# Kernel optimization log

Measured on AMD Instinct MI355X. Metric: run time of the kernel, lower is better.

## Reference

```python
import jax, jax.numpy as jnp
import numpy as np
from jax import lax

B, S, T = 512, 256, 10      # batch, src len, max_len (decoder steps)
V, E, H = 28, 32, 128       # vocab, embed, hidden
PAD = 0


def setup_inputs():
    key = jax.random.key(0)
    ks = jax.random.split(key, 16)
    k = 1.0 / np.sqrt(H)

    def u(kk, shape):
        return jax.random.uniform(kk, shape, jnp.float32, -k, k)

    embed = jax.random.normal(ks[0], (V, E), jnp.float32) * 0.02
    embed = embed.at[PAD].set(0.0)  # padding_idx=0 row is zero
    return dict(
        src=jax.random.randint(ks[1], (B, S), 0, V),
        target=jax.random.randint(ks[2], (B, T), 0, V),
        embed=embed,
        # PyTorch LSTM bias b = b_ih + b_hh folded into one vector (same math)
        enc_Wih_f=u(ks[3], (4 * H, E)), enc_Whh_f=u(ks[4], (4 * H, H)), enc_b_f=u(ks[5], (4 * H,)),
        enc_Wih_b=u(ks[6], (4 * H, E)), enc_Whh_b=u(ks[7], (4 * H, H)), enc_b_b=u(ks[8], (4 * H,)),
        dec_Wih=u(ks[9], (4 * H, E)), dec_Whh=u(ks[10], (4 * H, H)), dec_b=u(ks[11], (4 * H,)),
        proj_W=u(ks[12], (H, 2 * H)), proj_b=jnp.zeros((H,), jnp.float32),
        attn_W=u(ks[13], (H, 2 * H)), attn_b=jnp.zeros((H,), jnp.float32),
        out_W=u(ks[14], (V, H)), out_b=jnp.zeros((V,), jnp.float32),
    )


def _cell(h, c, xg, Whh):
    # PyTorch LSTMCell gate order: i, f, g, o
    g = xg + h @ Whh.T
    i, f, gg, o = jnp.split(g, 4, axis=-1)
    c = jax.nn.sigmoid(f) * c + jax.nn.sigmoid(i) * jnp.tanh(gg)
    return jax.nn.sigmoid(o) * jnp.tanh(c), c


def _run_lstm(x_emb, Wih, Whh, b):
    # precompute input projections for all steps: [S, B, 4H]
    xg = jnp.einsum('bse,ge->sbg', x_emb, Wih) + b
    h0 = jnp.zeros((x_emb.shape[0], Whh.shape[1]), x_emb.dtype)

    def step(carry, xg_t):
        h, c = _cell(carry[0], carry[1], xg_t, Whh)
        return (h, c), h

    (h, c), hs = lax.scan(step, (h0, h0), xg)
    return jnp.transpose(hs, (1, 0, 2)), h, c  # [B,S,H], [B,H], [B,H]


def _forward(src, target, embed, enc_Wih_f, enc_Whh_f, enc_b_f,
             enc_Wih_b, enc_Whh_b, enc_b_b, dec_Wih, dec_Whh, dec_b,
             proj_W, proj_b, attn_W, attn_b, out_W, out_b):
    src_emb = embed[src]  # [B,S,E]
    hs_f, hf, cf = _run_lstm(src_emb, enc_Wih_f, enc_Whh_f, enc_b_f)
    hs_r, hb, cb = _run_lstm(src_emb[:, ::-1], enc_Wih_b, enc_Whh_b, enc_b_b)
    enc_out = jnp.concatenate([hs_f, hs_r[:, ::-1]], axis=-1)  # [B,S,2H]
    h0, c0 = hf + hb, cf + cb  # sum over directions (num_layers=1)
    enc_proj = jnp.einsum('bsd,hd->bsh', enc_out, proj_W) + proj_b  # [B,S,H]

    # teacher forcing with ratio=1.0: decoder input tokens = [PAD, target[:, :-1]]
    dec_tok = jnp.concatenate(
        [jnp.full((src.shape[0], 1), PAD, target.dtype), target[:, :T - 1]], axis=1)
    xg_dec = jnp.einsum('bte,ge->tbg', embed[dec_tok], dec_Wih) + dec_b  # [T,B,4H]

    def dstep(carry, xg_t):
        h, c = _cell(carry[0], carry[1], xg_t, dec_Whh)
        scores = jnp.einsum('bsh,bh->bs', enc_proj, h)
        aw = jax.nn.softmax(scores, axis=1)
        ctx = jnp.einsum('bs,bsh->bh', aw, enc_proj)
        comb = jnp.tanh(jnp.concatenate([h, ctx], axis=1) @ attn_W.T + attn_b)
        logits = comb @ out_W.T + out_b
        return (h, c), logits

    _, logits = lax.scan(dstep, (h0, c0), xg_dec)  # [T,B,V]
    return jnp.transpose(logits, (1, 0, 2))  # [B,T,V]


def reference(src, target, embed, enc_Wih_f, enc_Whh_f, enc_b_f,
              enc_Wih_b, enc_Whh_b, enc_b_b, dec_Wih, dec_Whh, dec_b,
              proj_W, proj_b, attn_W, attn_b, out_W, out_b):
    return _forward(src, target, embed, enc_Wih_f, enc_Whh_f, enc_b_f,
                    enc_Wih_b, enc_Whh_b, enc_b_b, dec_Wih, dec_Whh, dec_b,
                    proj_W, proj_b, attn_W, attn_b, out_W, out_b)
```

## Files before the change

kernel.cpp:

```cpp
#include <hip/hip_runtime.h>
#include <hip/hip_bf16.h>
#include <stdint.h>

typedef unsigned short ushort_t;
typedef unsigned int uint_t;
typedef __attribute__((ext_vector_type(8))) short bfrag;
typedef __attribute__((ext_vector_type(4))) float f32x4;

#define B_ 512
#define S_ 256
#define T_ 10
#define V_ 28
#define H_ 128

#define XTD 0
#define XTG 14336
#define WTD 43008
#define AWT 108544
#define OWT 141312
#define PWT 144896
#define WPK 177664
#define HFIN 308736
#define CFIN 439808
#define HDEC 570880
#define HS_BYTE_OFF (1226240ull * 4ull)
#define PREP_N 308736

__device__ __forceinline__ float fast_exp2(float x) { return __builtin_amdgcn_exp2f(x); }
__device__ __forceinline__ float fast_rcp(float x)  { return __builtin_amdgcn_rcpf(x); }
__device__ __forceinline__ float sigm(float x) {
    return fast_rcp(1.f + fast_exp2(-1.4426950408889634f * x));
}
__device__ __forceinline__ float tanh_(float x) {
    return 1.f - 2.f * fast_rcp(1.f + fast_exp2(2.8853900817779268f * x));
}
__device__ __forceinline__ ushort_t f2bf(float x) {
    uint_t u = __float_as_uint(x);
    return (ushort_t)((u + 0x7FFFu + ((u >> 16) & 1u)) >> 16);
}
__device__ __forceinline__ float bflo(uint_t u) { return __uint_as_float(u << 16); }
__device__ __forceinline__ float bfhi(uint_t u) { return __uint_as_float(u & 0xFFFF0000u); }

__device__ __forceinline__ void lds_barrier() {
    asm volatile("s_waitcnt lgkmcnt(0)" ::: "memory");
    __builtin_amdgcn_s_barrier();
    __builtin_amdgcn_sched_barrier(0);
}

__global__ __launch_bounds__(256) void prep_kernel(
    const float* __restrict__ embed,
    const float* __restrict__ Wih_f, const float* __restrict__ b_f,
    const float* __restrict__ Wih_b, const float* __restrict__ b_b,
    const float* __restrict__ Wih_d, const float* __restrict__ b_d,
    const float* __restrict__ Whh_f, const float* __restrict__ Whh_b,
    const float* __restrict__ Whh_d,
    const float* __restrict__ attn_W, const float* __restrict__ out_W,
    const float* __restrict__ proj_W,
    float* __restrict__ ws)
{
    int i = blockIdx.x * 256 + threadIdx.x;
    if (i < XTG) {
        int v = i >> 9, q = i & 511;
        int uu = q >> 2, g = q & 3;
        int jj = g * 128 + uu;
        float acc = b_d[jj];
        #pragma unroll
        for (int e = 0; e < 32; ++e) acc = fmaf(embed[v * 32 + e], Wih_d[jj * 32 + e], acc);
        ws[XTD + i] = acc;
    } else if (i < WTD) {
        int r = i - XTG; int d = r / 14336; int rem = r % 14336;
        int v = rem >> 9, q = rem & 511;
        int uu = q >> 2, g = q & 3;
        int jj = g * 128 + uu;
        const float* Wih = d ? Wih_b : Wih_f;
        const float* bb  = d ? b_b   : b_f;
        float acc = bb[jj];
        #pragma unroll
        for (int e = 0; e < 32; ++e) acc = fmaf(embed[v * 32 + e], Wih[jj * 32 + e], acc);
        ws[XTG + r] = acc;
    } else if (i < AWT) {
        ws[i] = 0.f;
    } else if (i < OWT) {
        int r = i - AWT; int k = r >> 7, uu = r & 127;
        ws[i] = attn_W[uu * 256 + k];
    } else if (i < PWT) {
        int r = i - OWT; int k = r / 28, v = r % 28;
        ws[i] = out_W[v * 128 + k];
    } else if (i < WPK) {
        int r = i - PWT; int k = r >> 7, uu = r & 127;
        ws[i] = proj_W[uu * 256 + k];
    } else {
        int i2 = (i - WPK) * 2;
        #pragma unroll
        for (int p = 0; p < 2; ++p, ++i2) {
            if (i2 < 131072) {
                int e  = i2 & 7;
                int ll = (i2 >> 3) & 63;
                int kt = (i2 >> 9) & 3;
                int ni = (i2 >> 11) & 3;
                int wv = (i2 >> 13) & 7;
                int d  = (i2 >> 16) & 1;
                int jj = (ni * 8 + wv) * 16 + (ll & 15);
                int kp = kt * 32 + ((ll >> 4) << 3) + e;
                const float* Whh = d ? Whh_b : Whh_f;
                ((ushort_t*)(ws + WPK))[i2] = f2bf(Whh[jj * 128 + kp]);
            } else if (i2 < 196608) {
                int j2 = i2 - 131072;
                int e  = j2 & 7;
                int ll = (j2 >> 3) & 63;
                int kt = (j2 >> 9) & 3;
                int ni = (j2 >> 11) & 3;
                int wv = (j2 >> 13) & 7;
                int jj = (ni * 8 + wv) * 16 + (ll & 15);
                int kp = kt * 32 + ((ll >> 4) << 3) + e;
                ((ushort_t*)(ws + WPK))[i2] = f2bf(Whh_d[jj * 128 + kp]);
            }
        }
    }
}

__global__ __launch_bounds__(512, 2) void enc_kernel(
    const int* __restrict__ src,
    const float* __restrict__ xtg_base,
    const ushort_t* __restrict__ wpk,
    float* __restrict__ hfin, float* __restrict__ cfin,
    ushort_t* __restrict__ hs)
{
    const int bx = blockIdx.x;
    const int dir = bx >> 7;
    const int b0 = (bx & 127) << 2;
    const int tid = threadIdx.x;
    const int w = tid >> 6, l = tid & 63;
    const int lg = l >> 4, col = l & 15;
    const int u = (w << 4) + col;
    const int row = lg;

    __shared__ __align__(16) ushort_t hb[2][4][144];
    __shared__ __align__(16) int tokl[256][4];

    for (int i = tid; i < 1024; i += 512)
        tokl[i >> 2][i & 3] = src[(b0 + (i & 3)) * S_ + (i >> 2)];
    for (int i = tid; i < 576; i += 512) ((uint_t*)hb)[i] = 0u;

    const float* xtg = xtg_base + dir * 14336;

    bfrag bf[4][4];
    {
        const ushort_t* wb = wpk + (((size_t)dir * 8 + w) << 13) + l * 8;
        #pragma unroll
        for (int ni = 0; ni < 4; ++ni)
            #pragma unroll
            for (int kt = 0; kt < 4; ++kt)
                bf[ni][kt] = *reinterpret_cast<const bfrag*>(wb + ((ni * 4 + kt) << 9));
    }
    __syncthreads();

    float c_reg = 0.f, h_reg = 0.f;

    f32x4 xg_cur, xg_next;
    {
        int p0 = dir ? (S_ - 1) : 0;
        xg_cur = *reinterpret_cast<const f32x4*>(xtg + ((size_t)tokl[p0][row] << 9) + (u << 2));
    }

    const bfrag zf = {0, 0, 0, 0, 0, 0, 0, 0};
    bfrag af0 = zf, af1 = zf, af2 = zf, af3 = zf;
    const bool ard = ((col & 3) == 0);
    const int ar = col >> 2;
    const int swz = ar << 3;
    const f32x4 zacc = {0.f, 0.f, 0.f, 0.f};

    ushort_t* hs_ptr = hs + ((size_t)(b0 + row) * S_ + (dir ? (S_ - 1) : 0)) * 256
                          + dir * 128 + u;
    const int hs_step = dir ? -256 : 256;

    for (int t = 0; t < S_; ++t) {
        const int cb = t & 1, nb = cb ^ 1;

        if (t + 1 < S_) {
            int pn = dir ? (S_ - 2 - t) : (t + 1);
            xg_next = *reinterpret_cast<const f32x4*>(xtg + ((size_t)tokl[pn][row] << 9) + (u << 2));
        }

        if (ard) {
            const ushort_t* hp = &hb[cb][ar][0];
            af0 = *reinterpret_cast<const bfrag*>(hp + ((  0 + (lg << 3)) ^ swz));
            af1 = *reinterpret_cast<const bfrag*>(hp + (( 32 + (lg << 3)) ^ swz));
            af2 = *reinterpret_cast<const bfrag*>(hp + (( 64 + (lg << 3)) ^ swz));
            af3 = *reinterpret_cast<const bfrag*>(hp + (( 96 + (lg << 3)) ^ swz));
        }

        f32x4 a0 = __builtin_amdgcn_mfma_f32_16x16x32_bf16(af0, bf[0][0], zacc, 0, 0, 0);
        f32x4 a1 = __builtin_amdgcn_mfma_f32_16x16x32_bf16(af0, bf[1][0], zacc, 0, 0, 0);
        f32x4 a2 = __builtin_amdgcn_mfma_f32_16x16x32_bf16(af0, bf[2][0], zacc, 0, 0, 0);
        f32x4 a3 = __builtin_amdgcn_mfma_f32_16x16x32_bf16(af0, bf[3][0], zacc, 0, 0, 0);
        #define KT1(AF, kt) { \
            a0 = __builtin_amdgcn_mfma_f32_16x16x32_bf16(AF, bf[0][kt], a0, 0, 0, 0); \
            a1 = __builtin_amdgcn_mfma_f32_16x16x32_bf16(AF, bf[1][kt], a1, 0, 0, 0); \
            a2 = __builtin_amdgcn_mfma_f32_16x16x32_bf16(AF, bf[2][kt], a2, 0, 0, 0); \
            a3 = __builtin_amdgcn_mfma_f32_16x16x32_bf16(AF, bf[3][kt], a3, 0, 0, 0); \
        }
        KT1(af1, 1) KT1(af2, 2) KT1(af3, 3)
        #undef KT1

        {
            float gi = a0[0] + xg_cur[0], gf = a1[0] + xg_cur[1];
            float gg = a2[0] + xg_cur[2], go = a3[0] + xg_cur[3];
            float ii = sigm(gi), ff = sigm(gf), gG = tanh_(gg), oo = sigm(go);
            c_reg = ff * c_reg + ii * gG;
            float h = oo * tanh_(c_reg);
            h_reg = h;
            ushort_t hi = f2bf(h);
            hb[nb][row][u ^ (row << 3)] = hi;
            *hs_ptr = hi;
            hs_ptr += hs_step;
        }
        xg_cur = xg_next;
        lds_barrier();
    }

    hfin[dir * 65536 + (b0 + row) * 128 + u] = h_reg;
    cfin[dir * 65536 + (b0 + row) * 128 + u] = c_reg;
}

__global__ __launch_bounds__(512, 2) void dec_kernel(
    const int* __restrict__ target,
    const float* __restrict__ xtd_gi,
    const ushort_t* __restrict__ wpk,
    const float* __restrict__ hfin, const float* __restrict__ cfin,
    float* __restrict__ hdec)
{
    const int b0 = blockIdx.x << 2;
    const int tid = threadIdx.x;
    const int w = tid >> 6, l = tid & 63;
    const int lg = l >> 4, col = l & 15;
    const int u = (w << 4) + col;
    const int row = lg;

    __shared__ __align__(16) ushort_t hb[2][4][144];
    __shared__ __align__(16) int tokl[T_][4];

    if (tid < 40) {
        int t = tid >> 2, r = tid & 3;
        tokl[t][r] = (t == 0) ? 0 : target[(b0 + r) * T_ + t - 1];
    }

    bfrag bf[4][4];
    {
        const ushort_t* wb = wpk + 131072 + ((size_t)w << 13) + l * 8;
        #pragma unroll
        for (int ni = 0; ni < 4; ++ni)
            #pragma unroll
            for (int kt = 0; kt < 4; ++kt)
                bf[ni][kt] = *reinterpret_cast<const bfrag*>(wb + ((ni * 4 + kt) << 9));
    }

    float c_reg, h_reg;
    {
        int gb = (b0 + row) * 128 + u;
        h_reg = hfin[gb] + hfin[65536 + gb];
        c_reg = cfin[gb] + cfin[65536 + gb];
        hb[0][row][u ^ (row << 3)] = f2bf(h_reg);
    }
    __syncthreads();

    const bfrag zf = {0, 0, 0, 0, 0, 0, 0, 0};
    bfrag af0 = zf, af1 = zf, af2 = zf, af3 = zf;
    const bool ard = ((col & 3) == 0);
    const int ar = col >> 2;
    const int swz = ar << 3;
    const f32x4 zacc = {0.f, 0.f, 0.f, 0.f};

    for (int t = 0; t < T_; ++t) {
        const int cb = t & 1, nb = cb ^ 1;

        f32x4 xgc = *reinterpret_cast<const f32x4*>(
            xtd_gi + ((size_t)tokl[t][row] << 9) + (u << 2));

        if (ard) {
            const ushort_t* hp = &hb[cb][ar][0];
            af0 = *reinterpret_cast<const bfrag*>(hp + ((  0 + (lg << 3)) ^ swz));
            af1 = *reinterpret_cast<const bfrag*>(hp + (( 32 + (lg << 3)) ^ swz));
            af2 = *reinterpret_cast<const bfrag*>(hp + (( 64 + (lg << 3)) ^ swz));
            af3 = *reinterpret_cast<const bfrag*>(hp + (( 96 + (lg << 3)) ^ swz));
        }

        f32x4 a0 = __builtin_amdgcn_mfma_f32_16x16x32_bf16(af0, bf[0][0], zacc, 0, 0, 0);
        f32x4 a1 = __builtin_amdgcn_mfma_f32_16x16x32_bf16(af0, bf[1][0], zacc, 0, 0, 0);
        f32x4 a2 = __builtin_amdgcn_mfma_f32_16x16x32_bf16(af0, bf[2][0], zacc, 0, 0, 0);
        f32x4 a3 = __builtin_amdgcn_mfma_f32_16x16x32_bf16(af0, bf[3][0], zacc, 0, 0, 0);
        #define KT1(AF, kt) { \
            a0 = __builtin_amdgcn_mfma_f32_16x16x32_bf16(AF, bf[0][kt], a0, 0, 0, 0); \
            a1 = __builtin_amdgcn_mfma_f32_16x16x32_bf16(AF, bf[1][kt], a1, 0, 0, 0); \
            a2 = __builtin_amdgcn_mfma_f32_16x16x32_bf16(AF, bf[2][kt], a2, 0, 0, 0); \
            a3 = __builtin_amdgcn_mfma_f32_16x16x32_bf16(AF, bf[3][kt], a3, 0, 0, 0); \
        }
        KT1(af1, 1) KT1(af2, 2) KT1(af3, 3)
        #undef KT1

        {
            float gi = a0[0] + xgc[0], gf = a1[0] + xgc[1];
            float gg = a2[0] + xgc[2], go = a3[0] + xgc[3];
            float ii = sigm(gi), ff = sigm(gf), gG = tanh_(gg), oo = sigm(go);
            c_reg = ff * c_reg + ii * gG;
            float h = oo * tanh_(c_reg);
            h_reg = h;
            hb[nb][row][u ^ (row << 3)] = f2bf(h);
            hdec[((size_t)(b0 + row) * T_ + t) * 128 + u] = h;
        }
        lds_barrier();
    }
}

#define ESW(unit, row) ((((unit) ^ ((row) & 31))) << 3)
__global__ __launch_bounds__(512, 1) void attn_kernel(
    const float* __restrict__ hdec,
    const float* __restrict__ projW, const float* __restrict__ proj_b,
    const float* __restrict__ projWT,
    const float* __restrict__ attn_WT, const float* __restrict__ attn_b,
    const float* __restrict__ out_WT, const float* __restrict__ out_b,
    const ushort_t* __restrict__ hs, float* __restrict__ out)
{
    const int b = blockIdx.x;
    const int tid = threadIdx.x;

    __shared__ __align__(16) char smem[156672];
    ushort_t* e_lds = (ushort_t*)smem;
    float* hd   = (float*)(smem + 131072);
    float* q    = (float*)(smem + 136192);
    float* sc   = (float*)(smem + 146432);
    float* part = (float*)smem;
    float* wsum = (float*)(smem + 40960);

    const ushort_t* e = hs + (size_t)b * 65536;

    uint4 st[16];
    #pragma unroll
    for (int i = 0; i < 16; ++i)
        st[i] = *reinterpret_cast<const uint4*>(e + (i * 512 + tid) * 8);

    for (int i = tid; i < 1280; i += 512) hd[i] = hdec[(size_t)b * 1280 + i];
    lds_barrier();

    {
        const int half = tid >> 8, d = tid & 255;
        float acc[5];
        #pragma unroll
        for (int i = 0; i < 5; ++i) acc[i] = 0.f;
        for (int k = 0; k < 128; ++k) {
            float pw = projW[k * 256 + d];
            #pragma unroll
            for (int i = 0; i < 5; ++i) acc[i] = fmaf(hd[(half * 5 + i) * 128 + k], pw, acc[i]);
        }
        int swd = d ^ ((((uint_t)d >> 5) & 7) << 2);
        #pragma unroll
        for (int i = 0; i < 5; ++i) q[(half * 5 + i) * 256 + swd] = acc[i];
    }

    #pragma unroll
    for (int i = 0; i < 16; ++i) {
        int idx = i * 512 + tid;
        int row = idx >> 5, c = idx & 31;
        *reinterpret_cast<uint4*>(e_lds + row * 256 + ESW(c, row)) = st[i];
    }
    lds_barrier();

    {
        const int w = tid >> 6, l = tid & 63;
        const int s3 = l >> 3, k8 = l & 7;
        uint4 E0[4], E1[4], E2[4], E3[4];
        #pragma unroll
        for (int p = 0; p < 4; ++p) {
            int s = w * 32 + p * 8 + s3;
            const ushort_t* lrow = e_lds + s * 256;
            E0[p] = *reinterpret_cast<const uint4*>(lrow + ESW((k8 << 2) + 0, s));
            E1[p] = *reinterpret_cast<const uint4*>(lrow + ESW((k8 << 2) + 1, s));
            E2[p] = *reinterpret_cast<const uint4*>(lrow + ESW((k8 << 2) + 2, s));
            E3[p] = *reinterpret_cast<const uint4*>(lrow + ESW((k8 << 2) + 3, s));
        }
        for (int t = 0; t < 10; ++t) {
            const float* qb = &q[t * 256];
            #define QCH(i) (*reinterpret_cast<const float4*>(&qb[(k8 * 32 + (i) * 4) ^ (k8 << 2)]))
            float4 Q0 = QCH(0), Q1 = QCH(1), Q2 = QCH(2), Q3 = QCH(3);
            float4 Q4 = QCH(4), Q5 = QCH(5), Q6 = QCH(6), Q7 = QCH(7);
            #undef QCH
            #pragma unroll
            for (int p = 0; p < 4; ++p) {
                float a = 0.f;
                #define DOT4(pa, pb, qv) { float4 q_ = (qv); \
                    a = fmaf(bflo(pa), q_.x, a); a = fmaf(bfhi(pa), q_.y, a); \
                    a = fmaf(bflo(pb), q_.z, a); a = fmaf(bfhi(pb), q_.w, a); }
                DOT4(E0[p].x, E0[p].y, Q0); DOT4(E0[p].z, E0[p].w, Q1);
                DOT4(E1[p].x, E1[p].y, Q2); DOT4(E1[p].z, E1[p].w, Q3);
                DOT4(E2[p].x, E2[p].y, Q4); DOT4(E2[p].z, E2[p].w, Q5);
                DOT4(E3[p].x, E3[p].y, Q6); DOT4(E3[p].z, E3[p].w, Q7);
                #undef DOT4
                a += __shfl_xor(a, 1);
                a += __shfl_xor(a, 2);
                a += __shfl_xor(a, 4);
                if (k8 == 0) sc[t * 256 + (w * 32 + p * 8 + s3)] = a;
            }
        }
    }
    __syncthreads();

    {
        const int w = tid >> 6, l = tid & 63;
        for (int t = w; t < 10; t += 8) {
            float4 sv = *reinterpret_cast<const float4*>(&sc[t * 256 + l * 4]);
            float m = fmaxf(fmaxf(sv.x, sv.y), fmaxf(sv.z, sv.w));
            #pragma unroll
            for (int o = 1; o < 64; o <<= 1) m = fmaxf(m, __shfl_xor(m, o));
            float e0 = fast_exp2((sv.x - m) * 1.4426950408889634f);
            float e1 = fast_exp2((sv.y - m) * 1.4426950408889634f);
            float e2 = fast_exp2((sv.z - m) * 1.4426950408889634f);
            float e3 = fast_exp2((sv.w - m) * 1.4426950408889634f);
            float ssum = e0 + e1 + e2 + e3;
            #pragma unroll
            for (int o = 1; o < 64; o <<= 1) ssum += __shfl_xor(ssum, o);
            float inv = fast_rcp(ssum);
            *reinterpret_cast<float4*>(&sc[t * 256 + l * 4]) =
                make_float4(e0 * inv, e1 * inv, e2 * inv, e3 * inv);
        }
    }
    __syncthreads();

    {
        const int w = tid >> 6, l = tid & 63;
        const int chunk = w >> 1, tH = (w & 1) * 5;
        const int sbase = chunk * 64;
        const int unit = l >> 1, half2 = (l & 1) << 2;
        float ax[5], ay[5], az[5], aw2[5];
        #pragma unroll
        for (int i = 0; i < 5; ++i) { ax[i] = 0.f; ay[i] = 0.f; az[i] = 0.f; aw2[i] = 0.f; }
        for (int c4 = 0; c4 < 16; ++c4) {
            int s0 = sbase + c4 * 4;
            uint2 eA = *reinterpret_cast<const uint2*>(e_lds + (s0 + 0) * 256 + ESW(unit, s0 + 0) + half2);
            uint2 eB = *reinterpret_cast<const uint2*>(e_lds + (s0 + 1) * 256 + ESW(unit, s0 + 1) + half2);
            uint2 eC = *reinterpret_cast<const uint2*>(e_lds + (s0 + 2) * 256 + ESW(unit, s0 + 2) + half2);
            uint2 eD = *reinterpret_cast<const uint2*>(e_lds + (s0 + 3) * 256 + ESW(unit, s0 + 3) + half2);
            #pragma unroll
            for (int i = 0; i < 5; ++i) {
                float4 a4 = *reinterpret_cast<const float4*>(&sc[(tH + i) * 256 + s0]);
                ax[i]  = fmaf(bflo(eA.x), a4.x, ax[i]);  ay[i]  = fmaf(bfhi(eA.x), a4.x, ay[i]);
                az[i]  = fmaf(bflo(eA.y), a4.x, az[i]);  aw2[i] = fmaf(bfhi(eA.y), a4.x, aw2[i]);
                ax[i]  = fmaf(bflo(eB.x), a4.y, ax[i]);  ay[i]  = fmaf(bfhi(eB.x), a4.y, ay[i]);
                az[i]  = fmaf(bflo(eB.y), a4.y, az[i]);  aw2[i] = fmaf(bfhi(eB.y), a4.y, aw2[i]);
                ax[i]  = fmaf(bflo(eC.x), a4.z, ax[i]);  ay[i]  = fmaf(bfhi(eC.x), a4.z, ay[i]);
                az[i]  = fmaf(bflo(eC.y), a4.z, az[i]);  aw2[i] = fmaf(bfhi(eC.y), a4.z, aw2[i]);
                ax[i]  = fmaf(bflo(eD.x), a4.w, ax[i]);  ay[i]  = fmaf(bfhi(eD.x), a4.w, ay[i]);
                az[i]  = fmaf(bflo(eD.y), a4.w, az[i]);  aw2[i] = fmaf(bfhi(eD.y), a4.w, aw2[i]);
            }
        }
        __syncthreads();
        #pragma unroll
        for (int i = 0; i < 5; ++i)
            *reinterpret_cast<float4*>(&part[(chunk * 10 + tH + i) * 256 + l * 4]) =
                make_float4(ax[i], ay[i], az[i], aw2[i]);
    }
    __syncthreads();

    for (int i = tid; i < 2560; i += 512)
        wsum[i] = part[i] + part[2560 + i] + part[5120 + i] + part[7680 + i];
    if (tid < 512) wsum[2560 + tid] = 0.f;
    __syncthreads();

    {
        const int u = tid & 127, th = tid >> 7;
        const int st5 = (th < 2) ? th * 3 : 6 + (th - 2) * 2;
        const int cn = (th < 2) ? 3 : 2;
        float acc[3];
        #pragma unroll
        for (int i = 0; i < 3; ++i) acc[i] = proj_b[u];
        for (int k = 0; k < 256; ++k) {
            float pw = projWT[k * 128 + u];
            #pragma unroll
            for (int i = 0; i < 3; ++i) acc[i] = fmaf(pw, wsum[(st5 + i) * 256 + k], acc[i]);
        }
        #pragma unroll
        for (int i = 0; i < 3; ++i)
            if (i < cn) q[(st5 + i) * 128 + u] = acc[i];
    }
    __syncthreads();

    {
        const int u = tid & 127, th = tid >> 7;
        const int st6 = (th < 2) ? th * 3 : 6 + (th - 2) * 2;
        const int cn = (th < 2) ? 3 : 2;
        float acc[3];
        #pragma unroll
        for (int i = 0; i < 3; ++i) acc[i] = attn_b[u];
        for (int k = 0; k < 128; ++k) {
            float a1 = attn_WT[k * 128 + u];
            #pragma unroll
            for (int i = 0; i < 3; ++i) {
                int tt = (st6 + i < 10) ? (st6 + i) : 9;
                acc[i] = fmaf(a1, hd[tt * 128 + k], acc[i]);
            }
        }
        for (int k = 0; k < 128; ++k) {
            float a2 = attn_WT[(128 + k) * 128 + u];
            #pragma unroll
            for (int i = 0; i < 3; ++i) {
                int tt = (st6 + i < 10) ? (st6 + i) : 9;
                acc[i] = fmaf(a2, q[tt * 128 + k], acc[i]);
            }
        }
        #pragma unroll
        for (int i = 0; i < 3; ++i)
            if (i < cn) q[1280 + (st6 + i) * 128 + u] = tanh_(acc[i]);
    }
    __syncthreads();

    for (int o = tid; o < 280; o += 512) {
        int t = o / 28, v = o - t * 28;
        float acc = out_b[v];
        #pragma unroll 4
        for (int k = 0; k < 128; ++k)
            acc = fmaf(out_WT[k * 28 + v], q[1280 + t * 128 + k], acc);
        out[(size_t)b * 280 + o] = acc;
    }
}

extern "C" void kernel_launch(void* const* d_in, const int* in_sizes, int n_in,
                              void* d_out, int out_size, void* d_ws, size_t ws_size,
                              hipStream_t stream) {
    const int* src      = (const int*)d_in[0];
    const int* target   = (const int*)d_in[1];
    const float* embed  = (const float*)d_in[2];
    const float* Wih_f  = (const float*)d_in[3];
    const float* Whh_f  = (const float*)d_in[4];
    const float* b_f    = (const float*)d_in[5];
    const float* Wih_b  = (const float*)d_in[6];
    const float* Whh_b  = (const float*)d_in[7];
    const float* b_b    = (const float*)d_in[8];
    const float* Wih_d  = (const float*)d_in[9];
    const float* Whh_d  = (const float*)d_in[10];
    const float* b_d    = (const float*)d_in[11];
    const float* proj_W = (const float*)d_in[12];
    const float* proj_b = (const float*)d_in[13];
    const float* attn_W = (const float*)d_in[14];
    const float* attn_b = (const float*)d_in[15];
    const float* out_W  = (const float*)d_in[16];
    const float* out_b  = (const float*)d_in[17];

    float* ws = (float*)d_ws;
    ushort_t* hs = (ushort_t*)((char*)d_ws + HS_BYTE_OFF);
    float* out = (float*)d_out;

    prep_kernel<<<(PREP_N + 255) / 256, 256, 0, stream>>>(
        embed, Wih_f, b_f, Wih_b, b_b, Wih_d, b_d,
        Whh_f, Whh_b, Whh_d, attn_W, out_W, proj_W, ws);

    enc_kernel<<<256, 512, 0, stream>>>(
        src, ws + XTG, (const ushort_t*)(ws + WPK),
        ws + HFIN, ws + CFIN, hs);

    dec_kernel<<<128, 512, 0, stream>>>(
        target, ws + XTD, (const ushort_t*)(ws + WPK),
        ws + HFIN, ws + CFIN, ws + HDEC);

    attn_kernel<<<512, 512, 0, stream>>>(
        ws + HDEC, proj_W, proj_b, ws + PWT, ws + AWT, attn_b,
        ws + OWT, out_b, hs, out);
}
```

Before: 264.6 us.

## Precompute LDS fragment pointers, raise MFMA priority, fuse attn h-half into projection loop

In the encoder recurrence, the swizzled LDS read and write addresses for both double-buffer halves are computed once before the loop and chosen per step with a select. The MFMA chain is wrapped in s_setprio so the wave gets issue priority during the matmul. In the attention tail, the h-half of the attn_W product is folded into the projection loop and stored in an sc buffer, so the next phase only runs the ctx half. This trades extra registers and a new LDS buffer for less address arithmetic and fewer serial loop passes.

Result: faster. 254.6 us (-3.8%).

```diff
diff --git a/kernel.cpp b/kernel.cpp
--- a/kernel.cpp
+++ b/kernel.cpp
@@ -170,12 +170,22 @@
     const int swz = ar << 3;
     const f32x4 zacc = {0.f, 0.f, 0.f, 0.f};
 
+    const ushort_t* ap0[4]; const ushort_t* ap1[4];
+    #pragma unroll
+    for (int kt = 0; kt < 4; ++kt) {
+        int off = ((kt << 5) + (lg << 3)) ^ swz;
+        ap0[kt] = &hb[0][ar][0] + off;
+        ap1[kt] = &hb[1][ar][0] + off;
+    }
+    ushort_t* const hw0 = &hb[0][row][u ^ (row << 3)];
+    ushort_t* const hw1 = &hb[1][row][u ^ (row << 3)];
+
     ushort_t* hs_ptr = hs + ((size_t)(b0 + row) * S_ + (dir ? (S_ - 1) : 0)) * 256
                           + dir * 128 + u;
     const int hs_step = dir ? -256 : 256;
 
     for (int t = 0; t < S_; ++t) {
-        const int cb = t & 1, nb = cb ^ 1;
+        const int cb = t & 1;
 
         if (t + 1 < S_) {
             int pn = dir ? (S_ - 2 - t) : (t + 1);
@@ -183,13 +193,13 @@
         }
 
         if (ard) {
-            const ushort_t* hp = &hb[cb][ar][0];
-            af0 = *reinterpret_cast<const bfrag*>(hp + ((  0 + (lg << 3)) ^ swz));
-            af1 = *reinterpret_cast<const bfrag*>(hp + (( 32 + (lg << 3)) ^ swz));
-            af2 = *reinterpret_cast<const bfrag*>(hp + (( 64 + (lg << 3)) ^ swz));
-            af3 = *reinterpret_cast<const bfrag*>(hp + (( 96 + (lg << 3)) ^ swz));
-        }
-
+            af0 = *reinterpret_cast<const bfrag*>(cb ? ap1[0] : ap0[0]);
+            af1 = *reinterpret_cast<const bfrag*>(cb ? ap1[1] : ap0[1]);
+            af2 = *reinterpret_cast<const bfrag*>(cb ? ap1[2] : ap0[2]);
+            af3 = *reinterpret_cast<const bfrag*>(cb ? ap1[3] : ap0[3]);
+        }
+
+        __builtin_amdgcn_s_setprio(1);
         f32x4 a0 = __builtin_amdgcn_mfma_f32_16x16x32_bf16(af0, bf[0][0], zacc, 0, 0, 0);
         f32x4 a1 = __builtin_amdgcn_mfma_f32_16x16x32_bf16(af0, bf[1][0], zacc, 0, 0, 0);
         f32x4 a2 = __builtin_amdgcn_mfma_f32_16x16x32_bf16(af0, bf[2][0], zacc, 0, 0, 0);
@@ -202,6 +212,7 @@
         }
         KT1(af1, 1) KT1(af2, 2) KT1(af3, 3)
         #undef KT1
+        __builtin_amdgcn_s_setprio(0);
 
         {
             float gi = a0[0] + xg_cur[0], gf = a1[0] + xg_cur[1];
@@ -211,7 +222,7 @@
             float h = oo * tanh_(c_reg);
             h_reg = h;
             ushort_t hi = f2bf(h);
-            hb[nb][row][u ^ (row << 3)] = hi;
+            *(cb ? hw0 : hw1) = hi;
             *hs_ptr = hi;
             hs_ptr += hs_step;
         }
@@ -469,17 +480,27 @@
         const int u = tid & 127, th = tid >> 7;
         const int st5 = (th < 2) ? th * 3 : 6 + (th - 2) * 2;
         const int cn = (th < 2) ? 3 : 2;
-        float acc[3];
-        #pragma unroll
-        for (int i = 0; i < 3; ++i) acc[i] = proj_b[u];
-        for (int k = 0; k < 256; ++k) {
-            float pw = projWT[k * 128 + u];
-            #pragma unroll
-            for (int i = 0; i < 3; ++i) acc[i] = fmaf(pw, wsum[(st5 + i) * 256 + k], acc[i]);
+        float acc[3], accc[3];
+        #pragma unroll
+        for (int i = 0; i < 3; ++i) { acc[i] = proj_b[u]; accc[i] = attn_b[u]; }
+        for (int k = 0; k < 128; ++k) {
+            float pw1 = projWT[k * 128 + u];
+            float pw2 = projWT[(128 + k) * 128 + u];
+            float a1 = attn_WT[k * 128 + u];
+            #pragma unroll
+            for (int i = 0; i < 3; ++i) {
+                int tt = (st5 + i < 10) ? (st5 + i) : 9;
+                acc[i] = fmaf(pw1, wsum[(st5 + i) * 256 + k], acc[i]);
+                acc[i] = fmaf(pw2, wsum[(st5 + i) * 256 + 128 + k], acc[i]);
+                accc[i] = fmaf(a1, hd[tt * 128 + k], accc[i]);
+            }
         }
         #pragma unroll
         for (int i = 0; i < 3; ++i)
-            if (i < cn) q[(st5 + i) * 128 + u] = acc[i];
+            if (i < cn) {
+                q[(st5 + i) * 128 + u] = acc[i];
+                sc[(st5 + i) * 128 + u] = accc[i];
+            }
     }
     __syncthreads();
 
@@ -489,14 +510,9 @@
         const int cn = (th < 2) ? 3 : 2;
         float acc[3];
         #pragma unroll
-        for (int i = 0; i < 3; ++i) acc[i] = attn_b[u];
-        for (int k = 0; k < 128; ++k) {
-            float a1 = attn_WT[k * 128 + u];
-            #pragma unroll
-            for (int i = 0; i < 3; ++i) {
-                int tt = (st6 + i < 10) ? (st6 + i) : 9;
-                acc[i] = fmaf(a1, hd[tt * 128 + k], acc[i]);
-            }
+        for (int i = 0; i < 3; ++i) {
+            int tt = (st6 + i < 10) ? (st6 + i) : 9;
+            acc[i] = sc[tt * 128 + u];
         }
         for (int k = 0; k < 128; ++k) {
             float a2 = attn_WT[(128 + k) * 128 + u];
```
